# Kernel tuning notes

Hardware: AMD Instinct MI355X
Metric: run time of the kernel (lower is better)

Reference implementation:

```python
import jax, jax.numpy as jnp
import numpy as np

D = 512      # d_encoder
H = 8        # num_attn_heads
DH = 64      # d_attn
B = 8
S = 1024


def setup_inputs() -> dict:
    key = jax.random.key(0)
    ks = jax.random.split(key, 12)
    lim_in = 1.0 / np.sqrt(D)
    inp = {
        "Q": jax.random.normal(ks[0], (B, S, D), dtype=jnp.float32),
        "K": jax.random.normal(ks[1], (B, S, D), dtype=jnp.float32),
        "V": jax.random.normal(ks[2], (B, S, D), dtype=jnp.float32),
        # per-head projection weights stacked over heads: [H, D, DH]
        "Wq": jax.random.uniform(ks[3], (H, D, DH), jnp.float32, -lim_in, lim_in),
        "bq": jax.random.uniform(ks[4], (H, DH), jnp.float32, -lim_in, lim_in),
        "Wk": jax.random.uniform(ks[5], (H, D, DH), jnp.float32, -lim_in, lim_in),
        "bk": jax.random.uniform(ks[6], (H, DH), jnp.float32, -lim_in, lim_in),
        "Wv": jax.random.uniform(ks[7], (H, D, DH), jnp.float32, -lim_in, lim_in),
        "bv": jax.random.uniform(ks[8], (H, DH), jnp.float32, -lim_in, lim_in),
        "Wo": jax.random.uniform(ks[9], (D, D), jnp.float32, -lim_in, lim_in),
        "bo": jax.random.uniform(ks[10], (D,), jnp.float32, -lim_in, lim_in),
    }
    return inp


def reference(Q, K, V, Wq, bq, Wk, bk, Wv, bv, Wo, bo):
    scale = 1.0 / np.sqrt(DH).astype(np.float32)
    # per-head projections (the torch loop over heads, batched): [B,H,S,DH]
    Qh = jnp.einsum("bsd,hde->bhse", Q, Wq) + bq[None, :, None, :]
    Kh = jnp.einsum("bsd,hde->bhse", K, Wk) + bk[None, :, None, :]
    Vh = jnp.einsum("bsd,hde->bhse", V, Wv) + bv[None, :, None, :]
    # scaled dot-product attention with materialized scores [B,H,S,S]
    scores = jnp.einsum("bhse,bhte->bhst", Qh, Kh) * scale
    probs = jax.nn.softmax(scores, axis=-1)
    x = jnp.einsum("bhst,bhte->bhse", probs, Vh)  # [B,H,S,DH]
    # NOTE: original torch code does x.view(B, S, H*DH) directly on the
    # (B,H,S,DH) contiguous tensor WITHOUT transposing heads/time; we
    # faithfully replicate that memory-layout reshape.
    x = x.reshape(B, S, H * DH)
    x = x @ Wo + bo
    # dropout p=0.0 (p_drop set to 0 for deterministic reference)
    return x
```

## Files before the change

kernel.cpp:

```cpp
#include <hip/hip_runtime.h>
#include <hip/hip_bf16.h>

#define D_ENC 512
#define NH 8
#define DHD 64
#define BB 8
#define SS 1024

typedef unsigned short u16;
typedef __attribute__((ext_vector_type(8))) short short8;
typedef __attribute__((ext_vector_type(4))) float floatx4;

__device__ inline u16 f2bf(float f) {
    __hip_bfloat16 h = __float2bfloat16(f);
    return *reinterpret_cast<u16*>(&h);
}

__device__ inline void glds16(const u16* g, u16* l) {
    __builtin_amdgcn_global_load_lds(
        (const __attribute__((address_space(1))) void*)g,
        (__attribute__((address_space(3))) void*)l, 16, 0, 0);
}

__global__ __launch_bounds__(256) void prep_weights(
    const float* __restrict__ Wq, const float* __restrict__ Wk,
    const float* __restrict__ Wv, const float* __restrict__ Wo,
    u16* __restrict__ WqT, u16* __restrict__ WkT, u16* __restrict__ WvT,
    u16* __restrict__ WoT)
{
    int tid = blockIdx.x * 256 + threadIdx.x;
    const int WSZ = NH * D_ENC * DHD;
    if (tid < 3 * WSZ) {
        int wi = tid / WSZ, r = tid % WSZ;
        int d = r & 511;
        int e = (r >> 9) & 63;
        int h = r >> 15;
        const float* src = wi == 0 ? Wq : (wi == 1 ? Wk : Wv);
        u16* dst = wi == 0 ? WqT : (wi == 1 ? WkT : WvT);
        dst[r] = f2bf(src[h * (D_ENC * DHD) + d * DHD + e]);
    } else {
        int r = tid - 3 * WSZ;
        int d = r & 511, n = r >> 9;
        WoT[r] = f2bf(Wo[d * D_ENC + n]);
    }
}

__global__ __launch_bounds__(256) void convert_x(
    const float* __restrict__ Q, const float* __restrict__ K,
    const float* __restrict__ V, u16* __restrict__ Xbf)
{
    int t = blockIdx.x * 256 + threadIdx.x;
    int p = t / 524288, i = t % 524288;
    const float* src = p == 0 ? Q : (p == 1 ? K : V);
    const float4* s4 = reinterpret_cast<const float4*>(src) + (size_t)i * 2;
    float4 a = s4[0], b = s4[1];
    u16 hv[8] = { f2bf(a.x), f2bf(a.y), f2bf(a.z), f2bf(a.w),
                  f2bf(b.x), f2bf(b.y), f2bf(b.z), f2bf(b.w) };
    *reinterpret_cast<uint4*>(Xbf + (size_t)t * 8) =
        *reinterpret_cast<const uint4*>(hv);
}

__global__ __launch_bounds__(256, 4) void qkv_gemm(
    const u16* __restrict__ X, const u16* __restrict__ WT,
    const float* __restrict__ bias, u16* __restrict__ out,
    int proj, float oscale)
{
    const int m0 = blockIdx.x * 128;
    const int n0 = blockIdx.y * 64;
    __shared__ __align__(16) char smem[(128 * 64 + 64 * 64) * 2];
    u16* As = (u16*)smem;
    u16* Bs = As + 128 * 64;
    u16* Ts = (u16*)smem;

    const int tid = threadIdx.x, lane = tid & 63, w = tid >> 6;
    const int q = lane >> 4, l15 = lane & 15;
    const int lr = lane >> 3;
    const int lc = (lane & 7) ^ (lr & 7);

    floatx4 acc[2][4] = {};

    for (int d0 = 0; d0 < D_ENC; d0 += 64) {
        #pragma unroll
        for (int j = 0; j < 4; ++j) {
            int r = (j * 4 + w) * 8 + lr;
            glds16(X + (size_t)(m0 + r) * D_ENC + d0 + lc * 8,
                   As + (j * 4 + w) * 512);
        }
        #pragma unroll
        for (int j = 0; j < 2; ++j) {
            int r = (j * 4 + w) * 8 + lr;
            glds16(WT + (size_t)(n0 + r) * D_ENC + d0 + lc * 8,
                   Bs + (j * 4 + w) * 512);
        }
        __syncthreads();
        #pragma unroll
        for (int ks = 0; ks < 2; ++ks) {
            const int co = ((ks * 4 + q) ^ (l15 & 7)) * 8;
            short8 a0 = *(const short8*)&As[(32 * w + l15) * 64 + co];
            short8 a1 = *(const short8*)&As[(32 * w + 16 + l15) * 64 + co];
            #pragma unroll
            for (int f = 0; f < 4; ++f) {
                short8 bf = *(const short8*)&Bs[(f * 16 + l15) * 64 + co];
                acc[0][f] = __builtin_amdgcn_mfma_f32_16x16x32_bf16(a0, bf, acc[0][f], 0, 0, 0);
                acc[1][f] = __builtin_amdgcn_mfma_f32_16x16x32_bf16(a1, bf, acc[1][f], 0, 0, 0);
            }
        }
        __syncthreads();
    }

    const int b = m0 >> 10, sb = m0 & 1023, h = n0 >> 6;
    if (proj < 2) {
        u16* dst = out + ((size_t)(b * NH + h) * SS + sb) * DHD;
        #pragma unroll
        for (int i = 0; i < 2; ++i)
            #pragma unroll
            for (int f = 0; f < 4; ++f) {
                float bv = bias[n0 + f * 16 + l15];
                #pragma unroll
                for (int r = 0; r < 4; ++r)
                    dst[(32 * w + 16 * i + q * 4 + r) * DHD + f * 16 + l15] =
                        f2bf((acc[i][f][r] + bv) * oscale);
            }
    } else {
        #pragma unroll
        for (int i = 0; i < 2; ++i)
            #pragma unroll
            for (int f = 0; f < 4; ++f) {
                float bv = bias[n0 + f * 16 + l15];
                #pragma unroll
                for (int r = 0; r < 4; ++r)
                    Ts[(f * 16 + l15) * 136 + 32 * w + 16 * i + q * 4 + r] =
                        f2bf(acc[i][f][r] + bv);
            }
        __syncthreads();
        u16* dst = out + (size_t)(b * NH + h) * DHD * SS + sb;
        #pragma unroll
        for (int p2 = 0; p2 < 4; ++p2) {
            int c = (tid + 256 * p2) * 8;
            int e = c >> 7, s = c & 127;
            uint4 v = *(const uint4*)&Ts[e * 136 + s];
            *(uint4*)&dst[(size_t)e * SS + s] = v;
        }
    }
}

__global__ __launch_bounds__(256, 4) void flash_attn(
    const u16* __restrict__ Qh, const u16* __restrict__ Kh,
    const u16* __restrict__ VhT, u16* __restrict__ Xb)
{
    const int s0 = blockIdx.x * 64;
    const int h = blockIdx.y, b = blockIdx.z;
    const size_t bh = (size_t)(b * NH + h);

    __shared__ __align__(16) u16 Qs[64 * 64], Ks[64 * 64], Vs[64 * 64];
    __shared__ __align__(16) u16 Ps[64 * 72];

    const int tid = threadIdx.x, lane = tid & 63, w = tid >> 6;
    const int q = lane >> 4, l15 = lane & 15;
    const int lr = lane >> 3, lc = (lane & 7) ^ (lr & 7);

    const u16* qsrc = Qh + (bh * SS + s0) * DHD;
    #pragma unroll
    for (int j = 0; j < 2; ++j) {
        int r = (j * 4 + w) * 8 + lr;
        glds16(qsrc + r * DHD + lc * 8, Qs + (j * 4 + w) * 512);
    }

    floatx4 O[4] = {};
    floatx4 L = {0.f, 0.f, 0.f, 0.f};
    const short8 ones = {16256, 16256, 16256, 16256,
                         16256, 16256, 16256, 16256};

    for (int kt = 0; kt < SS / 64; ++kt) {
        const int k0 = kt * 64;
        const u16* ksrc = Kh + (bh * SS + k0) * DHD;
        const u16* vsrc = VhT + bh * DHD * SS + k0;
        #pragma unroll
        for (int j = 0; j < 2; ++j) {
            int r = (j * 4 + w) * 8 + lr;
            glds16(ksrc + r * DHD + lc * 8, Ks + (j * 4 + w) * 512);
            glds16(vsrc + (size_t)r * SS + lc * 8, Vs + (j * 4 + w) * 512);
        }
        __syncthreads();

        floatx4 sacc[4] = {};
        #pragma unroll
        for (int ks = 0; ks < 2; ++ks) {
            const int co = ((ks * 4 + q) ^ (l15 & 7)) * 8;
            short8 a = *(const short8*)&Qs[(16 * w + l15) * 64 + co];
            #pragma unroll
            for (int f = 0; f < 4; ++f) {
                short8 kb = *(const short8*)&Ks[(f * 16 + l15) * 64 + co];
                sacc[f] = __builtin_amdgcn_mfma_f32_16x16x32_bf16(a, kb, sacc[f], 0, 0, 0);
            }
        }

        #pragma unroll
        for (int f = 0; f < 4; ++f)
            #pragma unroll
            for (int r = 0; r < 4; ++r)
                Ps[(16 * w + q * 4 + r) * 72 + f * 16 + l15] =
                    f2bf(__expf(sacc[f][r]));

        #pragma unroll
        for (int ks = 0; ks < 2; ++ks) {
            short8 pa = *(const short8*)&Ps[(16 * w + l15) * 72 + ks * 32 + q * 8];
            L = __builtin_amdgcn_mfma_f32_16x16x32_bf16(pa, ones, L, 0, 0, 0);
            const int co = ((ks * 4 + q) ^ (l15 & 7)) * 8;
            #pragma unroll
            for (int f = 0; f < 4; ++f) {
                short8 vb = *(const short8*)&Vs[(f * 16 + l15) * 64 + co];
                O[f] = __builtin_amdgcn_mfma_f32_16x16x32_bf16(pa, vb, O[f], 0, 0, 0);
            }
        }
        __syncthreads();
    }

    u16* dst = Xb + (bh * SS + s0) * DHD;
    #pragma unroll
    for (int f = 0; f < 4; ++f)
        #pragma unroll
        for (int r = 0; r < 4; ++r)
            dst[(16 * w + q * 4 + r) * DHD + f * 16 + l15] =
                f2bf(O[f][r] / L[r]);
}

__global__ __launch_bounds__(256, 4) void out_gemm(
    const u16* __restrict__ X, const u16* __restrict__ WT,
    const float* __restrict__ bias, float* __restrict__ out)
{
    const int m0 = blockIdx.x * 128;
    const int n0 = blockIdx.y * 64;
    __shared__ __align__(16) u16 As[128 * 64];
    __shared__ __align__(16) u16 Bs[64 * 64];

    const int tid = threadIdx.x, lane = tid & 63, w = tid >> 6;
    const int q = lane >> 4, l15 = lane & 15;
    const int lr = lane >> 3, lc = (lane & 7) ^ (lr & 7);

    floatx4 acc[2][4] = {};

    for (int d0 = 0; d0 < D_ENC; d0 += 64) {
        #pragma unroll
        for (int j = 0; j < 4; ++j) {
            int r = (j * 4 + w) * 8 + lr;
            glds16(X + (size_t)(m0 + r) * D_ENC + d0 + lc * 8,
                   As + (j * 4 + w) * 512);
        }
        #pragma unroll
        for (int j = 0; j < 2; ++j) {
            int r = (j * 4 + w) * 8 + lr;
            glds16(WT + (size_t)(n0 + r) * D_ENC + d0 + lc * 8,
                   Bs + (j * 4 + w) * 512);
        }
        __syncthreads();
        #pragma unroll
        for (int ks = 0; ks < 2; ++ks) {
            const int co = ((ks * 4 + q) ^ (l15 & 7)) * 8;
            short8 a0 = *(const short8*)&As[(32 * w + l15) * 64 + co];
            short8 a1 = *(const short8*)&As[(32 * w + 16 + l15) * 64 + co];
            #pragma unroll
            for (int f = 0; f < 4; ++f) {
                short8 bf = *(const short8*)&Bs[(f * 16 + l15) * 64 + co];
                acc[0][f] = __builtin_amdgcn_mfma_f32_16x16x32_bf16(a0, bf, acc[0][f], 0, 0, 0);
                acc[1][f] = __builtin_amdgcn_mfma_f32_16x16x32_bf16(a1, bf, acc[1][f], 0, 0, 0);
            }
        }
        __syncthreads();
    }
    #pragma unroll
    for (int i = 0; i < 2; ++i)
        #pragma unroll
        for (int f = 0; f < 4; ++f) {
            float bv = bias[n0 + f * 16 + l15];
            #pragma unroll
            for (int r = 0; r < 4; ++r)
                out[(size_t)(m0 + 32 * w + 16 * i + q * 4 + r) * D_ENC +
                    n0 + f * 16 + l15] = acc[i][f][r] + bv;
        }
}

extern "C" void kernel_launch(void* const* d_in, const int* in_sizes, int n_in,
                              void* d_out, int out_size, void* d_ws, size_t ws_size,
                              hipStream_t stream)
{
    const float* Q  = (const float*)d_in[0];
    const float* K  = (const float*)d_in[1];
    const float* V  = (const float*)d_in[2];
    const float* Wq = (const float*)d_in[3];
    const float* bq = (const float*)d_in[4];
    const float* Wk = (const float*)d_in[5];
    const float* bk = (const float*)d_in[6];
    const float* Wv = (const float*)d_in[7];
    const float* bv = (const float*)d_in[8];
    const float* Wo = (const float*)d_in[9];
    const float* bo = (const float*)d_in[10];
    float* out = (float*)d_out;

    char* ws = (char*)d_ws;
    u16* WqT = (u16*)(ws + 0);
    u16* WkT = (u16*)(ws + 524288);
    u16* WvT = (u16*)(ws + 1048576);
    u16* WoT = (u16*)(ws + 1572864);
    u16* Xbf = (u16*)(ws + 2097152);
    u16* Kh  = (u16*)(ws + 2097152);
    u16* VhT = (u16*)(ws + 10485760);
    u16* Xb  = (u16*)(ws + 18874368);
    u16* Qh  = (u16*)(ws + 27262976);

    hipLaunchKernelGGL(prep_weights, dim3(4096), dim3(256), 0, stream,
                       Wq, Wk, Wv, Wo, WqT, WkT, WvT, WoT);
    hipLaunchKernelGGL(convert_x, dim3(6144), dim3(256), 0, stream,
                       Q, K, V, Xbf);
    hipLaunchKernelGGL(qkv_gemm, dim3(64, 8), dim3(256), 0, stream,
                       Xbf,           WqT, bq, Qh,  0, 0.125f);
    hipLaunchKernelGGL(qkv_gemm, dim3(64, 8), dim3(256), 0, stream,
                       Xbf + 4194304, WkT, bk, Kh,  1, 1.0f);
    hipLaunchKernelGGL(qkv_gemm, dim3(64, 8), dim3(256), 0, stream,
                       Xbf + 8388608, WvT, bv, VhT, 2, 1.0f);
    hipLaunchKernelGGL(flash_attn, dim3(16, 8, 8), dim3(256), 0, stream,
                       Qh, Kh, VhT, Xb);
    hipLaunchKernelGGL(out_gemm, dim3(64, 8), dim3(256), 0, stream,
                       Xb, WoT, bo, out);
}
```

Before: 194.1 us.

## Merge prep kernels, batch QKV GEMMs, double-buffer K/V in attention

Combines the weight and input conversion kernels into one launch and runs the three QKV projections as a single 3D grid, so there are fewer launches and one larger wave of blocks. In flash attention, Q fragments now live in registers, K/V tiles are double-buffered so the next tile's loads overlap compute, and P is written to a swizzled LDS layout with packed 4-element stores. The workspace layout is moved so Kh/VhT no longer alias Xbf, which the batched QKV launch requires. LDS use per block rises and only one barrier remains per iteration, which is an ordering risk.

```diff
diff --git a/kernel.cpp b/kernel.cpp
--- a/kernel.cpp
+++ b/kernel.cpp
@@ -22,49 +22,59 @@
         (__attribute__((address_space(3))) void*)l, 16, 0, 0);
 }
 
-__global__ __launch_bounds__(256) void prep_weights(
+__global__ __launch_bounds__(256) void prep_all(
     const float* __restrict__ Wq, const float* __restrict__ Wk,
     const float* __restrict__ Wv, const float* __restrict__ Wo,
+    const float* __restrict__ Q, const float* __restrict__ K,
+    const float* __restrict__ V,
     u16* __restrict__ WqT, u16* __restrict__ WkT, u16* __restrict__ WvT,
-    u16* __restrict__ WoT)
-{
-    int tid = blockIdx.x * 256 + threadIdx.x;
-    const int WSZ = NH * D_ENC * DHD;
-    if (tid < 3 * WSZ) {
-        int wi = tid / WSZ, r = tid % WSZ;
-        int d = r & 511;
-        int e = (r >> 9) & 63;
-        int h = r >> 15;
-        const float* src = wi == 0 ? Wq : (wi == 1 ? Wk : Wv);
-        u16* dst = wi == 0 ? WqT : (wi == 1 ? WkT : WvT);
-        dst[r] = f2bf(src[h * (D_ENC * DHD) + d * DHD + e]);
+    u16* __restrict__ WoT, u16* __restrict__ Xbf)
+{
+    int bx = blockIdx.x;
+    if (bx < 4096) {
+        int tid = bx * 256 + threadIdx.x;
+        const int WSZ = NH * D_ENC * DHD;
+        if (tid < 3 * WSZ) {
+            int wi = tid / WSZ, r = tid % WSZ;
+            int d = r & 511;
+            int e = (r >> 9) & 63;
+            int h = r >> 15;
+            const float* src = wi == 0 ? Wq : (wi == 1 ? Wk : Wv);
+            u16* dst = wi == 0 ? WqT : (wi == 1 ? WkT : WvT);
+            dst[r] = f2bf(src[h * (D_ENC * DHD) + d * DHD + e]);
+        } else {
+            int r = tid - 3 * WSZ;
+            int d = r & 511, n = r >> 9;
+            WoT[r] = f2bf(Wo[d * D_ENC + n]);
+        }
     } else {
-        int r = tid - 3 * WSZ;
-        int d = r & 511, n = r >> 9;
-        WoT[r] = f2bf(Wo[d * D_ENC + n]);
-    }
-}
-
-__global__ __launch_bounds__(256) void convert_x(
-    const float* __restrict__ Q, const float* __restrict__ K,
-    const float* __restrict__ V, u16* __restrict__ Xbf)
-{
-    int t = blockIdx.x * 256 + threadIdx.x;
-    int p = t / 524288, i = t % 524288;
-    const float* src = p == 0 ? Q : (p == 1 ? K : V);
-    const float4* s4 = reinterpret_cast<const float4*>(src) + (size_t)i * 2;
-    float4 a = s4[0], b = s4[1];
-    u16 hv[8] = { f2bf(a.x), f2bf(a.y), f2bf(a.z), f2bf(a.w),
-                  f2bf(b.x), f2bf(b.y), f2bf(b.z), f2bf(b.w) };
-    *reinterpret_cast<uint4*>(Xbf + (size_t)t * 8) =
-        *reinterpret_cast<const uint4*>(hv);
+        int t = (bx - 4096) * 256 + threadIdx.x;
+        int p = t / 524288, i = t % 524288;
+        const float* src = p == 0 ? Q : (p == 1 ? K : V);
+        const float4* s4 = reinterpret_cast<const float4*>(src) + (size_t)i * 2;
+        float4 a = s4[0], b = s4[1];
+        u16 hv[8] = { f2bf(a.x), f2bf(a.y), f2bf(a.z), f2bf(a.w),
+                      f2bf(b.x), f2bf(b.y), f2bf(b.z), f2bf(b.w) };
+        *reinterpret_cast<uint4*>(Xbf + (size_t)t * 8) =
+            *reinterpret_cast<const uint4*>(hv);
+    }
 }
 
 __global__ __launch_bounds__(256, 4) void qkv_gemm(
-    const u16* __restrict__ X, const u16* __restrict__ WT,
-    const float* __restrict__ bias, u16* __restrict__ out,
-    int proj, float oscale)
-{
+    const u16* __restrict__ Xbf,
+    const u16* __restrict__ WqT, const u16* __restrict__ WkT,
+    const u16* __restrict__ WvT,
+    const float* __restrict__ bq, const float* __restrict__ bk,
+    const float* __restrict__ bv,
+    u16* __restrict__ Qh, u16* __restrict__ Kh, u16* __restrict__ VhT)
+{
+    const int proj = blockIdx.z;
+    const u16* X = Xbf + (size_t)proj * (BB * SS * D_ENC);
+    const u16* WT = proj == 0 ? WqT : (proj == 1 ? WkT : WvT);
+    const float* bias = proj == 0 ? bq : (proj == 1 ? bk : bv);
+    u16* out = proj == 0 ? Qh : (proj == 1 ? Kh : VhT);
+    const float oscale = proj == 0 ? 0.125f : 1.0f;
+
     const int m0 = blockIdx.x * 128;
     const int n0 = blockIdx.y * 64;
     __shared__ __align__(16) char smem[(128 * 64 + 64 * 64) * 2];
@@ -115,22 +125,22 @@
         for (int i = 0; i < 2; ++i)
             #pragma unroll
             for (int f = 0; f < 4; ++f) {
-                float bv = bias[n0 + f * 16 + l15];
+                float bv_ = bias[n0 + f * 16 + l15];
                 #pragma unroll
                 for (int r = 0; r < 4; ++r)
                     dst[(32 * w + 16 * i + q * 4 + r) * DHD + f * 16 + l15] =
-                        f2bf((acc[i][f][r] + bv) * oscale);
+                        f2bf((acc[i][f][r] + bv_) * oscale);
             }
     } else {
         #pragma unroll
         for (int i = 0; i < 2; ++i)
             #pragma unroll
             for (int f = 0; f < 4; ++f) {
-                float bv = bias[n0 + f * 16 + l15];
+                float bv_ = bias[n0 + f * 16 + l15];
                 #pragma unroll
                 for (int r = 0; r < 4; ++r)
                     Ts[(f * 16 + l15) * 136 + 32 * w + 16 * i + q * 4 + r] =
-                        f2bf(acc[i][f][r] + bv);
+                        f2bf(acc[i][f][r] + bv_);
             }
         __syncthreads();
         u16* dst = out + (size_t)(b * NH + h) * DHD * SS + sb;
@@ -152,18 +162,24 @@
     const int h = blockIdx.y, b = blockIdx.z;
     const size_t bh = (size_t)(b * NH + h);
 
-    __shared__ __align__(16) u16 Qs[64 * 64], Ks[64 * 64], Vs[64 * 64];
-    __shared__ __align__(16) u16 Ps[64 * 72];
+    __shared__ __align__(16) u16 Ks[2][64 * 64], Vs[2][64 * 64], Ps[64 * 64];
 
     const int tid = threadIdx.x, lane = tid & 63, w = tid >> 6;
     const int q = lane >> 4, l15 = lane & 15;
     const int lr = lane >> 3, lc = (lane & 7) ^ (lr & 7);
 
-    const u16* qsrc = Qh + (bh * SS + s0) * DHD;
+    const u16* qrow = Qh + (bh * SS + s0 + 16 * w + l15) * DHD;
+    short8 qb0 = *(const short8*)(qrow + q * 8);
+    short8 qb1 = *(const short8*)(qrow + 32 + q * 8);
+
+    const u16* kbase = Kh + bh * SS * DHD;
+    const u16* vbase = VhT + bh * DHD * SS;
+
     #pragma unroll
     for (int j = 0; j < 2; ++j) {
         int r = (j * 4 + w) * 8 + lr;
-        glds16(qsrc + r * DHD + lc * 8, Qs + (j * 4 + w) * 512);
+        glds16(kbase + (size_t)r * DHD + lc * 8, Ks[0] + (j * 4 + w) * 512);
+        glds16(vbase + (size_t)r * SS + lc * 8, Vs[0] + (j * 4 + w) * 512);
     }
 
     floatx4 O[4] = {};
@@ -172,48 +188,56 @@
                          16256, 16256, 16256, 16256};
 
     for (int kt = 0; kt < SS / 64; ++kt) {
-        const int k0 = kt * 64;
-        const u16* ksrc = Kh + (bh * SS + k0) * DHD;
-        const u16* vsrc = VhT + bh * DHD * SS + k0;
-        #pragma unroll
-        for (int j = 0; j < 2; ++j) {
-            int r = (j * 4 + w) * 8 + lr;
-            glds16(ksrc + r * DHD + lc * 8, Ks + (j * 4 + w) * 512);
-            glds16(vsrc + (size_t)r * SS + lc * 8, Vs + (j * 4 + w) * 512);
-        }
-        __syncthreads();
+        __syncthreads();
+        if (kt + 1 < SS / 64) {
+            const int k1 = (kt + 1) * 64;
+            u16* kd = Ks[(kt + 1) & 1];
+            u16* vd = Vs[(kt + 1) & 1];
+            #pragma unroll
+            for (int j = 0; j < 2; ++j) {
+                int r = (j * 4 + w) * 8 + lr;
+                glds16(kbase + (size_t)(k1 + r) * DHD + lc * 8,
+                       kd + (j * 4 + w) * 512);
+                glds16(vbase + (size_t)r * SS + k1 + lc * 8,
+                       vd + (j * 4 + w) * 512);
+            }
+        }
+        const u16* ks_ = Ks[kt & 1];
+        const u16* vs_ = Vs[kt & 1];
 
         floatx4 sacc[4] = {};
+        #pragma unroll
+        for (int f = 0; f < 4; ++f) {
+            const int co0 = ((0 * 4 + q) ^ (l15 & 7)) * 8;
+            const int co1 = ((1 * 4 + q) ^ (l15 & 7)) * 8;
+            short8 ka0 = *(const short8*)&ks_[(f * 16 + l15) * 64 + co0];
+            short8 ka1 = *(const short8*)&ks_[(f * 16 + l15) * 64 + co1];
+            sacc[f] = __builtin_amdgcn_mfma_f32_16x16x32_bf16(ka0, qb0, sacc[f], 0, 0, 0);
+            sacc[f] = __builtin_amdgcn_mfma_f32_16x16x32_bf16(ka1, qb1, sacc[f], 0, 0, 0);
+        }
+
+        #pragma unroll
+        for (int f = 0; f < 4; ++f) {
+            ushort4 pk;
+            pk.x = f2bf(__expf(sacc[f][0]));
+            pk.y = f2bf(__expf(sacc[f][1]));
+            pk.z = f2bf(__expf(sacc[f][2]));
+            pk.w = f2bf(__expf(sacc[f][3]));
+            const int chunk = (2 * f + (q >> 1)) ^ (l15 & 7);
+            *(ushort4*)&Ps[(16 * w + l15) * 64 + chunk * 8 + (q & 1) * 4] = pk;
+        }
+
         #pragma unroll
         for (int ks = 0; ks < 2; ++ks) {
             const int co = ((ks * 4 + q) ^ (l15 & 7)) * 8;
-            short8 a = *(const short8*)&Qs[(16 * w + l15) * 64 + co];
-            #pragma unroll
-            for (int f = 0; f < 4; ++f) {
-                short8 kb = *(const short8*)&Ks[(f * 16 + l15) * 64 + co];
-                sacc[f] = __builtin_amdgcn_mfma_f32_16x16x32_bf16(a, kb, sacc[f], 0, 0, 0);
-            }
-        }
-
-        #pragma unroll
-        for (int f = 0; f < 4; ++f)
-            #pragma unroll
-            for (int r = 0; r < 4; ++r)
-                Ps[(16 * w + q * 4 + r) * 72 + f * 16 + l15] =
-                    f2bf(__expf(sacc[f][r]));
-
-        #pragma unroll
-        for (int ks = 0; ks < 2; ++ks) {
-            short8 pa = *(const short8*)&Ps[(16 * w + l15) * 72 + ks * 32 + q * 8];
+            short8 pa = *(const short8*)&Ps[(16 * w + l15) * 64 + co];
             L = __builtin_amdgcn_mfma_f32_16x16x32_bf16(pa, ones, L, 0, 0, 0);
-            const int co = ((ks * 4 + q) ^ (l15 & 7)) * 8;
-            #pragma unroll
-            for (int f = 0; f < 4; ++f) {
-                short8 vb = *(const short8*)&Vs[(f * 16 + l15) * 64 + co];
+            #pragma unroll
+            for (int f = 0; f < 4; ++f) {
+                short8 vb = *(const short8*)&vs_[(f * 16 + l15) * 64 + co];
                 O[f] = __builtin_amdgcn_mfma_f32_16x16x32_bf16(pa, vb, O[f], 0, 0, 0);
             }
         }
-        __syncthreads();
     }
 
     u16* dst = Xb + (bh * SS + s0) * DHD;
@@ -272,11 +296,11 @@
     for (int i = 0; i < 2; ++i)
         #pragma unroll
         for (int f = 0; f < 4; ++f) {
-            float bv = bias[n0 + f * 16 + l15];
+            float bv_ = bias[n0 + f * 16 + l15];
             #pragma unroll
             for (int r = 0; r < 4; ++r)
                 out[(size_t)(m0 + 32 * w + 16 * i + q * 4 + r) * D_ENC +
-                    n0 + f * 16 + l15] = acc[i][f][r] + bv;
+                    n0 + f * 16 + l15] = acc[i][f][r] + bv_;
         }
 }
 
@@ -303,21 +327,15 @@
     u16* WvT = (u16*)(ws + 1048576);
     u16* WoT = (u16*)(ws + 1572864);
     u16* Xbf = (u16*)(ws + 2097152);
-    u16* Kh  = (u16*)(ws + 2097152);
-    u16* VhT = (u16*)(ws + 10485760);
-    u16* Xb  = (u16*)(ws + 18874368);
+    u16* Xb  = (u16*)(ws + 2097152);
     u16* Qh  = (u16*)(ws + 27262976);
-
-    hipLaunchKernelGGL(prep_weights, dim3(4096), dim3(256), 0, stream,
-                       Wq, Wk, Wv, Wo, WqT, WkT, WvT, WoT);
-    hipLaunchKernelGGL(convert_x, dim3(6144), dim3(256), 0, stream,
-                       Q, K, V, Xbf);
-    hipLaunchKernelGGL(qkv_gemm, dim3(64, 8), dim3(256), 0, stream,
-                       Xbf,           WqT, bq, Qh,  0, 0.125f);
-    hipLaunchKernelGGL(qkv_gemm, dim3(64, 8), dim3(256), 0, stream,
-                       Xbf + 4194304, WkT, bk, Kh,  1, 1.0f);
-    hipLaunchKernelGGL(qkv_gemm, dim3(64, 8), dim3(256), 0, stream,
-                       Xbf + 8388608, WvT, bv, VhT, 2, 1.0f);
+    u16* Kh  = (u16*)(ws + 35651584);
+    u16* VhT = (u16*)(ws + 44040192);
+
+    hipLaunchKernelGGL(prep_all, dim3(10240), dim3(256), 0, stream,
+                       Wq, Wk, Wv, Wo, Q, K, V, WqT, WkT, WvT, WoT, Xbf);
+    hipLaunchKernelGGL(qkv_gemm, dim3(64, 8, 3), dim3(256), 0, stream,
+                       Xbf, WqT, WkT, WvT, bq, bk, bv, Qh, Kh, VhT);
     hipLaunchKernelGGL(flash_attn, dim3(16, 8, 8), dim3(256), 0, stream,
                        Qh, Kh, VhT, Xb);
     hipLaunchKernelGGL(out_gemm, dim3(64, 8), dim3(256), 0, stream,
```

After: 173.6 us. -10.5%, faster.
